# Kernel optimization log

Hardware: AMD Instinct MI355X
Metric: run time of the kernel (lower is better)

## Reference

```python
import jax, jax.numpy as jnp
import numpy as np

R = 32  # reduction channels

def _conv1x1(W, x):
    # W: [out, in], x: [b, in, h, w] -> [b, out, h, w]
    return jnp.einsum('oc,bchw->bohw', W, x)

def setup_inputs() -> dict:
    key = jax.random.key(0)
    ks = jax.random.split(key, 9)
    C, H, W = 512, 32, 32
    B = 64
    HW = H * W
    def w(k, o, i):
        return jax.random.normal(k, (o, i), dtype=jnp.float32) * (1.0 / np.sqrt(i))
    return {
        'x': jax.random.normal(ks[0], (B, C, H, W), dtype=jnp.float32),
        'W_reduce': w(ks[1], R, C),
        'W_restore': w(ks[2], C, R),
        'W_phi': w(ks[3], R, R),
        'W_theta': w(ks[4], R, R),
        'W_g': w(ks[5], R, R),
        'W_mask': w(ks[6], R, R),
        'pos_embedding': jax.random.normal(ks[7], (1, HW, HW), dtype=jnp.float32),
        'pos_embedding_decoder': jax.random.normal(ks[8], (1, R, H, W), dtype=jnp.float32),
    }

def reference(x, W_reduce, W_restore, W_phi, W_theta, W_g, W_mask, pos_embedding, pos_embedding_decoder):
    b, c, h, w = x.shape
    hw = h * w
    xr = _conv1x1(W_reduce, x)                               # [b, R, h, w]
    x_phi = _conv1x1(W_phi, xr).reshape(b, R, hw)            # [b, R, hw]
    x_theta = _conv1x1(W_theta, xr).reshape(b, R, hw).transpose(0, 2, 1)  # [b, hw, R]
    x_g = (_conv1x1(W_g, xr) + pos_embedding_decoder).reshape(b, R, hw).transpose(0, 2, 1)  # [b, hw, R]
    attention = jnp.einsum('bnr,brm->bnm', x_theta, x_phi) + pos_embedding  # [b, hw, hw]
    attention = jax.nn.softmax(attention, axis=-1)
    y = jnp.einsum('bnm,bmr->bnr', attention, x_g)           # [b, hw, R]
    y = y.transpose(0, 2, 1).reshape(b, R, h, w)
    y = _conv1x1(W_mask, y)
    y = _conv1x1(W_restore, y)
    return y + x
```

## Files before the change

kernel.cpp:

```cpp
#include <hip/hip_runtime.h>
#include <cstddef>

#define BATCH 64
#define CCH   512
#define RCH   32
#define HW    1024

typedef __attribute__((ext_vector_type(8))) _Float16 half8;
typedef __attribute__((ext_vector_type(4))) _Float16 half4v;
typedef __attribute__((ext_vector_type(4))) float f32x4;

__device__ inline uint pk2h(float a, float b) {
  auto h = __builtin_amdgcn_cvt_pkrtz(a, b);
  return __builtin_bit_cast(uint, h);
}
__device__ inline ushort h16(float f) {
  _Float16 h = (_Float16)f;
  return __builtin_bit_cast(ushort, h);
}

__device__ inline void gload16(const float* g, float* lds) {
  __builtin_amdgcn_global_load_lds((const __attribute__((address_space(1))) void*)g,
                                   (__attribute__((address_space(3))) void*)lds, 16, 0, 0);
}

__global__ __launch_bounds__(256) void k_prep(const float* __restrict__ Wred,
    const float* __restrict__ Wrest, const float* __restrict__ Wphi,
    const float* __restrict__ Wth,   const float* __restrict__ Wg,
    const float* __restrict__ Wmask, const float* __restrict__ pos,
    float* __restrict__ Wcomb, _Float16* __restrict__ Whf,
    uint2* __restrict__ posq) {
  const int blk = blockIdx.x;
  const int t = threadIdx.x;
  if (blk >= 256) {
    __shared__ ushort tile[64][68];
    int tb = blk - 256;
    int n0 = (tb >> 4) * 64, m0 = (tb & 15) * 64;
    int nl = t >> 2, c4 = t & 3;
    const float* src = &pos[(size_t)(n0 + nl) * HW + m0 + c4 * 16];
#pragma unroll
    for (int k = 0; k < 4; ++k) {
      float4 p = *(const float4*)(src + k * 4);
      ushort* d = &tile[nl][c4 * 16 + k * 4];
      d[0] = h16(p.x); d[1] = h16(p.y); d[2] = h16(p.z); d[3] = h16(p.w);
    }
    __syncthreads();
    int nl2 = t & 63, mq = t >> 6;
#pragma unroll
    for (int k = 0; k < 4; ++k) {
      int m4l = k * 4 + mq;
      const ushort* s = &tile[nl2][m4l * 4];
      uint2 o;
      o.x = (uint)s[0] | ((uint)s[1] << 16);
      o.y = (uint)s[2] | ((uint)s[3] << 16);
      posq[(size_t)(m0 / 4 + m4l) * HW + n0 + nl2] = o;
    }
    return;
  }
  int tid = blk * 256 + t;
  int job = tid >> 14, idx = tid & 16383;
  if (job == 0) {
    int co = idx >> 5, r = idx & 31;
    float a = 0.f;
#pragma unroll
    for (int rp = 0; rp < RCH; ++rp)
      a += Wrest[co * RCH + rp] * Wmask[rp * RCH + r];
    Wcomb[idx] = a;
  } else {
    const float* Wm = (job == 1) ? Wphi : (job == 2) ? Wth : Wg;
    int rp = idx >> 9, c = idx & 511;
    float a = 0.f;
#pragma unroll
    for (int r = 0; r < RCH; ++r)
      a += Wm[rp * RCH + r] * Wred[r * CCH + c];
    int kk = c >> 5, hl = (c >> 3) & 3, j = c & 7;
    int mix = job - 1, m = rp >> 4, ll = rp & 15;
    size_t off = ((((size_t)kk * 3 + mix) * 2 + m) * 64 + hl * 16 + ll) * 8 + j;
    Whf[off] = (_Float16)a;
  }
}

__global__ __launch_bounds__(256) void k_qkg(const float* __restrict__ x,
    const _Float16* __restrict__ Whf, const float* __restrict__ posdec,
    _Float16* __restrict__ phiT, _Float16* __restrict__ thT,
    _Float16* __restrict__ g) {
  __shared__ float buf[2][32][64];
  __shared__ float gt[4][32][17];

  const int t = threadIdx.x;
  const int wv = t >> 6, lane = t & 63;
  const int ll = lane & 15, hl = lane >> 4;
  const int b = blockIdx.y;
  const int px0b = blockIdx.x * 64;
  const f32x4 fz = {0.f, 0.f, 0.f, 0.f};

  f32x4 acc[3][2];
#pragma unroll
  for (int m1 = 0; m1 < 3; ++m1)
#pragma unroll
    for (int m2 = 0; m2 < 2; ++m2) acc[m1][m2] = fz;

  {
    const float* xbase = x + ((size_t)b * CCH) * HW + px0b;
#pragma unroll
    for (int rd = 0; rd < 2; ++rd) {
      int ch = rd * 16 + wv * 4 + (lane >> 4);
      gload16(xbase + (size_t)ch * HW + (lane & 15) * 4, &buf[0][rd * 16 + wv * 4][0]);
    }
  }
  __syncthreads();

  for (int kk = 0; kk < 16; ++kk) {
    const int cur = kk & 1;
    if (kk < 15) {
      const float* xbase = x + ((size_t)b * CCH + (kk + 1) * 32) * HW + px0b;
#pragma unroll
      for (int rd = 0; rd < 2; ++rd) {
        int ch = rd * 16 + wv * 4 + (lane >> 4);
        gload16(xbase + (size_t)ch * HW + (lane & 15) * 4, &buf[cur ^ 1][rd * 16 + wv * 4][0]);
      }
    }
    float xv[8];
#pragma unroll
    for (int j = 0; j < 8; ++j) xv[j] = buf[cur][hl * 8 + j][wv * 16 + ll];
    union { half8 h8; uint u[4]; } X;
    X.u[0] = pk2h(xv[0], xv[1]);
    X.u[1] = pk2h(xv[2], xv[3]);
    X.u[2] = pk2h(xv[4], xv[5]);
    X.u[3] = pk2h(xv[6], xv[7]);
#pragma unroll
    for (int mix = 0; mix < 3; ++mix)
#pragma unroll
      for (int m = 0; m < 2; ++m) {
        half8 wh = *(const half8*)&Whf[((((size_t)kk * 3 + mix) * 2 + m) * 64 + lane) * 8];
        acc[mix][m] = __builtin_amdgcn_mfma_f32_16x16x32_f16(wh, X.h8, acc[mix][m], 0, 0, 0);
      }
    __syncthreads();
  }

#pragma unroll
  for (int mix = 0; mix < 2; ++mix) {
    _Float16* outb = (mix ? thT : phiT) + ((size_t)b * HW + px0b + wv * 16) * 32;
#pragma unroll
    for (int m = 0; m < 2; ++m) {
      f32x4 v = acc[mix][m];
      uint2 o;
      o.x = pk2h(v[0], v[1]);
      o.y = pk2h(v[2], v[3]);
      *(uint2*)(outb + (size_t)ll * 32 + m * 16 + hl * 4) = o;
    }
  }

  __syncthreads();
#pragma unroll
  for (int m = 0; m < 2; ++m)
#pragma unroll
    for (int i = 0; i < 4; ++i)
      gt[wv][m * 16 + hl * 4 + i][ll] = acc[2][m][i];
  __syncthreads();
#pragma unroll
  for (int rr = 0; rr < 4; ++rr) {
    int r = rr * 8 + hl * 2 + (ll >> 3), p2 = (ll & 7) * 2;
    const float2 pd = *(const float2*)&posdec[(size_t)r * HW + px0b + wv * 16 + p2];
    uint pk = pk2h(gt[wv][r][p2] + pd.x, gt[wv][r][p2 + 1] + pd.y);
    *(uint*)&g[((size_t)b * RCH + r) * HW + px0b + wv * 16 + p2] = pk;
  }
}

__global__ __launch_bounds__(512) void k_attn(const _Float16* __restrict__ phiT,
    const _Float16* __restrict__ thT, const _Float16* __restrict__ g,
    const _Float16* __restrict__ posqh, float* __restrict__ y2) {
  __shared__ __align__(16) _Float16 slabm[8][16][72];

  const int t = threadIdx.x;
  const int wv = t >> 6, lane = t & 63;
  const int ll = lane & 15, hl = lane >> 4;
  const int b = blockIdx.y;
  const int nw = blockIdx.x * 128 + wv * 16;
  const f32x4 fz = {0.f, 0.f, 0.f, 0.f};

  const _Float16* phib = phiT + (size_t)b * (HW * 32);
  const _Float16* thb  = thT  + (size_t)b * (HW * 32);
  const _Float16* gb   = g    + (size_t)b * (RCH * HW);

  half8 th = *(const half8*)&thb[(size_t)(nw + ll) * 32 + hl * 8];

  f32x4 y[2] = {fz, fz};
  float m_run = -3e38f, s_run = 0.f;

  for (int ck = 0; ck < 8; ++ck) {
    const int mch = ck * 128;

    f32x4 acc[8];
#pragma unroll
    for (int mf = 0; mf < 8; ++mf) {
      half8 ph = *(const half8*)&phib[(size_t)(mch + mf * 16 + ll) * 32 + hl * 8];
      acc[mf] = __builtin_amdgcn_mfma_f32_16x16x32_f16(ph, th, fz, 0, 0, 0);
    }

#pragma unroll
    for (int mf = 0; mf < 8; ++mf) {
      half4v pp = *(const half4v*)&posqh[((size_t)(ck * 32 + mf * 4 + hl) * HW + nw + ll) * 4];
#pragma unroll
      for (int i = 0; i < 4; ++i) acc[mf][i] += (float)pp[i];
    }

    float mv = acc[0][0];
#pragma unroll
    for (int mf = 0; mf < 8; ++mf)
#pragma unroll
      for (int i = 0; i < 4; ++i) mv = fmaxf(mv, acc[mf][i]);
    mv = fmaxf(mv, __shfl_xor(mv, 16));
    mv = fmaxf(mv, __shfl_xor(mv, 32));
    float mnew = fmaxf(m_run, mv);
    float fac = __expf(m_run - mnew);
    m_run = mnew;
    float s_ = 0.f;
#pragma unroll
    for (int mf = 0; mf < 8; ++mf)
#pragma unroll
      for (int i = 0; i < 4; ++i) {
        float p = __expf(acc[mf][i] - mnew);
        acc[mf][i] = p;
        s_ += p;
      }
    s_ += __shfl_xor(s_, 16);
    s_ += __shfl_xor(s_, 32);
    s_run = s_run * fac + s_;
    y[0] *= fac;
    y[1] *= fac;

#pragma unroll
    for (int h = 0; h < 2; ++h) {
#pragma unroll
      for (int mf2 = 0; mf2 < 4; ++mf2) {
        f32x4 v = acc[h * 4 + mf2];
        uint2 w;
        w.x = pk2h(v[0], v[1]);
        w.y = pk2h(v[2], v[3]);
        *(uint2*)&slabm[wv][ll][mf2 * 16 + hl * 4] = w;
      }
      asm volatile("s_waitcnt lgkmcnt(0)" ::: "memory");
      __builtin_amdgcn_sched_barrier(0);
#pragma unroll
      for (int ks = 0; ks < 2; ++ks) {
        half8 bfr = *(const half8*)&slabm[wv][ll][ks * 32 + hl * 8];
#pragma unroll
        for (int rf = 0; rf < 2; ++rf) {
          half8 ag = *(const half8*)&gb[(size_t)(rf * 16 + ll) * HW + mch + h * 64 + ks * 32 + hl * 8];
          y[rf] = __builtin_amdgcn_mfma_f32_16x16x32_f16(ag, bfr, y[rf], 0, 0, 0);
        }
      }
      asm volatile("s_waitcnt lgkmcnt(0)" ::: "memory");
      __builtin_amdgcn_sched_barrier(0);
    }
  }

  float inv = 1.f / s_run;
#pragma unroll
  for (int rf = 0; rf < 2; ++rf)
#pragma unroll
    for (int i = 0; i < 4; ++i)
      y2[((size_t)b * RCH + rf * 16 + hl * 4 + i) * HW + nw + ll] = y[rf][i] * inv;
}

__global__ __launch_bounds__(256) void k_restore(const float* __restrict__ x,
    const float* __restrict__ Wcomb, const float* __restrict__ y2,
    float* __restrict__ out) {
  const int t = threadIdx.x;
  const int gp = blockIdx.x * 256 + t;
  const int b = gp >> 10, n = gp & 1023;
  const int co0 = blockIdx.y * 64;

  float yv[RCH];
  const float* y2b = y2 + ((size_t)b * RCH) * HW + n;
#pragma unroll
  for (int r = 0; r < RCH; ++r) yv[r] = y2b[(size_t)r * HW];

  const float* xb = x + ((size_t)b * CCH) * HW + n;
  float* ob = out + ((size_t)b * CCH) * HW + n;
  for (int co = co0; co < co0 + 64; ++co) {
    float a = xb[(size_t)co * HW];
#pragma unroll
    for (int qq = 0; qq < RCH; qq += 4) {
      const float4 w = *(const float4*)(Wcomb + co * RCH + qq);
      a += w.x * yv[qq] + w.y * yv[qq + 1] + w.z * yv[qq + 2] + w.w * yv[qq + 3];
    }
    ob[(size_t)co * HW] = a;
  }
}

extern "C" void kernel_launch(void* const* d_in, const int* in_sizes, int n_in,
                              void* d_out, int out_size, void* d_ws, size_t ws_size,
                              hipStream_t stream) {
  const float* x      = (const float*)d_in[0];
  const float* Wred   = (const float*)d_in[1];
  const float* Wrest  = (const float*)d_in[2];
  const float* Wphi   = (const float*)d_in[3];
  const float* Wth    = (const float*)d_in[4];
  const float* Wg     = (const float*)d_in[5];
  const float* Wmask  = (const float*)d_in[6];
  const float* pos    = (const float*)d_in[7];
  const float* posdec = (const float*)d_in[8];
  float* out = (float*)d_out;

  const size_t NE = (size_t)BATCH * RCH * HW;
  _Float16* phiT = (_Float16*)d_ws;
  _Float16* thT  = phiT + NE;
  _Float16* gbuf = thT + NE;
  float*    y2   = (float*)(gbuf + NE);
  float*    Wcomb = y2 + NE;
  _Float16* Whf  = (_Float16*)(Wcomb + CCH * RCH);
  _Float16* posqh = Whf + 3 * RCH * CCH;

  k_prep   <<<dim3(512),     dim3(256), 0, stream>>>(Wred, Wrest, Wphi, Wth, Wg, Wmask,
                                                     pos, Wcomb, Whf, (uint2*)posqh);
  k_qkg    <<<dim3(16, 64),  dim3(256), 0, stream>>>(x, Whf, posdec, phiT, thT, gbuf);
  k_attn   <<<dim3(8, 64),   dim3(512), 0, stream>>>(phiT, thT, gbuf, posqh, y2);
  k_restore<<<dim3(256, 8),  dim3(256), 0, stream>>>(x, Wcomb, y2, out);
}
```

Before: 137.9 us.

## Fuse restore 1x1 conv and residual into attention kernel; keep pos bias fp32

The separate restore kernel is removed. Its work (Wcomb·y plus x residual) now runs at the end of the attention kernel, which stages the normalized y in LDS. This drops the y2 global round trip and one launch. The positional bias is also kept in fp32 and fed straight in as the MFMA accumulator init, which removes the separate add loop but doubles the bias read traffic. Only 512 blocks now do the large 512-channel output write, each looping over 128 channels serially, so that phase has less parallelism and may be limited by latency.

```diff
diff --git a/kernel.cpp b/kernel.cpp
--- a/kernel.cpp
+++ b/kernel.cpp
@@ -7,16 +7,11 @@
 #define HW    1024
 
 typedef __attribute__((ext_vector_type(8))) _Float16 half8;
-typedef __attribute__((ext_vector_type(4))) _Float16 half4v;
 typedef __attribute__((ext_vector_type(4))) float f32x4;
 
 __device__ inline uint pk2h(float a, float b) {
   auto h = __builtin_amdgcn_cvt_pkrtz(a, b);
   return __builtin_bit_cast(uint, h);
-}
-__device__ inline ushort h16(float f) {
-  _Float16 h = (_Float16)f;
-  return __builtin_bit_cast(ushort, h);
 }
 
 __device__ inline void gload16(const float* g, float* lds) {
@@ -29,11 +24,11 @@
     const float* __restrict__ Wth,   const float* __restrict__ Wg,
     const float* __restrict__ Wmask, const float* __restrict__ pos,
     float* __restrict__ Wcomb, _Float16* __restrict__ Whf,
-    uint2* __restrict__ posq) {
+    float4* __restrict__ posf) {
   const int blk = blockIdx.x;
   const int t = threadIdx.x;
   if (blk >= 256) {
-    __shared__ ushort tile[64][68];
+    __shared__ float tile[64][69];
     int tb = blk - 256;
     int n0 = (tb >> 4) * 64, m0 = (tb & 15) * 64;
     int nl = t >> 2, c4 = t & 3;
@@ -41,19 +36,16 @@
 #pragma unroll
     for (int k = 0; k < 4; ++k) {
       float4 p = *(const float4*)(src + k * 4);
-      ushort* d = &tile[nl][c4 * 16 + k * 4];
-      d[0] = h16(p.x); d[1] = h16(p.y); d[2] = h16(p.z); d[3] = h16(p.w);
+      float* d = &tile[nl][c4 * 16 + k * 4];
+      d[0] = p.x; d[1] = p.y; d[2] = p.z; d[3] = p.w;
     }
     __syncthreads();
     int nl2 = t & 63, mq = t >> 6;
 #pragma unroll
     for (int k = 0; k < 4; ++k) {
       int m4l = k * 4 + mq;
-      const ushort* s = &tile[nl2][m4l * 4];
-      uint2 o;
-      o.x = (uint)s[0] | ((uint)s[1] << 16);
-      o.y = (uint)s[2] | ((uint)s[3] << 16);
-      posq[(size_t)(m0 / 4 + m4l) * HW + n0 + nl2] = o;
+      const float* s = &tile[nl2][m4l * 4];
+      posf[(size_t)(m0 / 4 + m4l) * HW + n0 + nl2] = make_float4(s[0], s[1], s[2], s[3]);
     }
     return;
   }
@@ -169,14 +161,17 @@
 
 __global__ __launch_bounds__(512) void k_attn(const _Float16* __restrict__ phiT,
     const _Float16* __restrict__ thT, const _Float16* __restrict__ g,
-    const _Float16* __restrict__ posqh, float* __restrict__ y2) {
+    const float* __restrict__ posf, const float* __restrict__ Wcomb,
+    const float* __restrict__ x, float* __restrict__ out) {
   __shared__ __align__(16) _Float16 slabm[8][16][72];
+  __shared__ float ynorm[RCH][132];
 
   const int t = threadIdx.x;
   const int wv = t >> 6, lane = t & 63;
   const int ll = lane & 15, hl = lane >> 4;
   const int b = blockIdx.y;
-  const int nw = blockIdx.x * 128 + wv * 16;
+  const int n0b = blockIdx.x * 128;
+  const int nw = n0b + wv * 16;
   const f32x4 fz = {0.f, 0.f, 0.f, 0.f};
 
   const _Float16* phib = phiT + (size_t)b * (HW * 32);
@@ -194,15 +189,9 @@
     f32x4 acc[8];
 #pragma unroll
     for (int mf = 0; mf < 8; ++mf) {
+      f32x4 pc = *(const f32x4*)&posf[((size_t)(ck * 32 + mf * 4 + hl) * HW + nw + ll) * 4];
       half8 ph = *(const half8*)&phib[(size_t)(mch + mf * 16 + ll) * 32 + hl * 8];
-      acc[mf] = __builtin_amdgcn_mfma_f32_16x16x32_f16(ph, th, fz, 0, 0, 0);
-    }
-
-#pragma unroll
-    for (int mf = 0; mf < 8; ++mf) {
-      half4v pp = *(const half4v*)&posqh[((size_t)(ck * 32 + mf * 4 + hl) * HW + nw + ll) * 4];
-#pragma unroll
-      for (int i = 0; i < 4; ++i) acc[mf][i] += (float)pp[i];
+      acc[mf] = __builtin_amdgcn_mfma_f32_16x16x32_f16(ph, th, pc, 0, 0, 0);
     }
 
     float mv = acc[0][0];
@@ -261,32 +250,27 @@
   for (int rf = 0; rf < 2; ++rf)
 #pragma unroll
     for (int i = 0; i < 4; ++i)
-      y2[((size_t)b * RCH + rf * 16 + hl * 4 + i) * HW + nw + ll] = y[rf][i] * inv;
-}
-
-__global__ __launch_bounds__(256) void k_restore(const float* __restrict__ x,
-    const float* __restrict__ Wcomb, const float* __restrict__ y2,
-    float* __restrict__ out) {
-  const int t = threadIdx.x;
-  const int gp = blockIdx.x * 256 + t;
-  const int b = gp >> 10, n = gp & 1023;
-  const int co0 = blockIdx.y * 64;
-
-  float yv[RCH];
-  const float* y2b = y2 + ((size_t)b * RCH) * HW + n;
-#pragma unroll
-  for (int r = 0; r < RCH; ++r) yv[r] = y2b[(size_t)r * HW];
-
-  const float* xb = x + ((size_t)b * CCH) * HW + n;
-  float* ob = out + ((size_t)b * CCH) * HW + n;
-  for (int co = co0; co < co0 + 64; ++co) {
-    float a = xb[(size_t)co * HW];
-#pragma unroll
-    for (int qq = 0; qq < RCH; qq += 4) {
-      const float4 w = *(const float4*)(Wcomb + co * RCH + qq);
-      a += w.x * yv[qq] + w.y * yv[qq + 1] + w.z * yv[qq + 2] + w.w * yv[qq + 3];
-    }
-    ob[(size_t)co * HW] = a;
+      ynorm[rf * 16 + hl * 4 + i][wv * 16 + ll] = y[rf][i] * inv;
+  __syncthreads();
+
+  {
+    const int nloc = t & 127, cq = t >> 7;
+    float yv[RCH];
+#pragma unroll
+    for (int r = 0; r < RCH; ++r) yv[r] = ynorm[r][nloc];
+    const float* xp = x + ((size_t)b * CCH + cq * 128) * HW + n0b + nloc;
+    float* op = out + ((size_t)b * CCH + cq * 128) * HW + n0b + nloc;
+    const float* wbase = Wcomb + cq * 128 * RCH;
+    for (int i = 0; i < 128; ++i) {
+      float a = xp[(size_t)i * HW];
+      const float* wr = wbase + i * RCH;
+#pragma unroll
+      for (int q = 0; q < RCH; q += 4) {
+        const float4 w = *(const float4*)(wr + q);
+        a += w.x * yv[q] + w.y * yv[q + 1] + w.z * yv[q + 2] + w.w * yv[q + 3];
+      }
+      op[(size_t)i * HW] = a;
+    }
   }
 }
 
@@ -308,14 +292,12 @@
   _Float16* phiT = (_Float16*)d_ws;
   _Float16* thT  = phiT + NE;
   _Float16* gbuf = thT + NE;
-  float*    y2   = (float*)(gbuf + NE);
-  float*    Wcomb = y2 + NE;
+  float*    Wcomb = (float*)(gbuf + NE);
   _Float16* Whf  = (_Float16*)(Wcomb + CCH * RCH);
-  _Float16* posqh = Whf + 3 * RCH * CCH;
-
-  k_prep   <<<dim3(512),     dim3(256), 0, stream>>>(Wred, Wrest, Wphi, Wth, Wg, Wmask,
-                                                     pos, Wcomb, Whf, (uint2*)posqh);
-  k_qkg    <<<dim3(16, 64),  dim3(256), 0, stream>>>(x, Whf, posdec, phiT, thT, gbuf);
-  k_attn   <<<dim3(8, 64),   dim3(512), 0, stream>>>(phiT, thT, gbuf, posqh, y2);
-  k_restore<<<dim3(256, 8),  dim3(256), 0, stream>>>(x, Wcomb, y2, out);
-}
+  float*    posf = (float*)(Whf + 3 * RCH * CCH);
+
+  k_prep <<<dim3(512),    dim3(256), 0, stream>>>(Wred, Wrest, Wphi, Wth, Wg, Wmask,
+                                                  pos, Wcomb, Whf, (float4*)posf);
+  k_qkg  <<<dim3(16, 64), dim3(256), 0, stream>>>(x, Whf, posdec, phiT, thT, gbuf);
+  k_attn <<<dim3(8, 64),  dim3(512), 0, stream>>>(phiT, thT, gbuf, posf, Wcomb, x, out);
+}
```

Result: slower. 219.4 us (+59.1%).
